# Kernel optimization log

Hardware: AMD Instinct MI355X
Metric: run time of the kernel (lower is better)

The kernel has to match this reference:

```python
import jax, jax.numpy as jnp
import numpy as np
from math import sqrt

B, S, D_MODEL = 2, 2048, 1024
H = 16
ADIM = D_MODEL // H  # 64
K_REL = 16
N_PEMB = 2 * K_REL + 1  # 33, bidirectional rel-pos vocabulary


def setup_inputs() -> dict:
    key = jax.random.key(0)
    ks = jax.random.split(key, 8)
    sc = 0.02
    return {
        "iQ": jax.random.normal(ks[0], (B, S, D_MODEL), jnp.float32),
        "iK": jax.random.normal(ks[1], (B, S, D_MODEL), jnp.float32),
        "iV": jax.random.normal(ks[2], (B, S, D_MODEL), jnp.float32),
        "Wq": jax.random.normal(ks[3], (D_MODEL, D_MODEL), jnp.float32) * sc,
        "Wk": jax.random.normal(ks[4], (D_MODEL, D_MODEL), jnp.float32) * sc,
        "Wv": jax.random.normal(ks[5], (D_MODEL, D_MODEL), jnp.float32) * sc,
        "Wo": jax.random.normal(ks[6], (D_MODEL, D_MODEL), jnp.float32) * sc,
        "rel_pemb": jax.random.normal(ks[7], (N_PEMB, ADIM), jnp.float32) * sc,
    }


def reference(iQ, iK, iV, Wq, Wk, Wv, Wo, rel_pemb):
    b, nq, _ = iQ.shape
    seql = iK.shape[1]
    # projections -> [b, h, len, d]
    q = (iQ @ Wq).reshape(b, nq, H, ADIM).transpose(0, 2, 1, 3)
    k = (iK @ Wk).reshape(b, seql, H, ADIM).transpose(0, 2, 1, 3)
    v = (iV @ Wv).reshape(b, seql, H, ADIM).transpose(0, 2, 1, 3)
    # content scores: [b, h, nq, seql]
    scores = jnp.einsum("bhqd,bhsd->bhqs", q, k)
    # relative position bias: rel[i, j] = clamp(j - i, -K, K) + K
    pos = jnp.arange(seql)
    rel = jnp.clip(pos[None, :] - pos[:, None], -K_REL, K_REL) + K_REL
    rel = rel[seql - nq:, :]  # narrow to query rows: [nq, seql]
    e = rel_pemb[rel]  # [nq, seql, d]
    scores = scores + jnp.einsum("bhqd,qsd->bhqs", q, e)
    scores = scores / sqrt(ADIM)
    attn = jax.nn.softmax(scores, axis=-1)
    ctx = jnp.einsum("bhqs,bhsd->bqhd", attn, v).reshape(b, nq, H * ADIM)
    return ctx @ Wo
```

## Files before the change

kernel.cpp:

```cpp
#include <hip/hip_runtime.h>
#include <hip/hip_bf16.h>

#define BB 2
#define S 2048
#define DM 1024
#define H 16
#define ADIM 64
#define NP 33

typedef __bf16 bf16x8 __attribute__((ext_vector_type(8)));
typedef __bf16 bf16x4 __attribute__((ext_vector_type(4)));
typedef float f32x4 __attribute__((ext_vector_type(4)));

__device__ __forceinline__ void gload16(const void* g, void* l) {
  __builtin_amdgcn_global_load_lds(
      (__attribute__((address_space(1))) void*)(g),
      (__attribute__((address_space(3))) void*)(l), 16, 0, 0);
}

__global__ __launch_bounds__(256) void tobf16(
    const float* __restrict__ X0, const float* __restrict__ X1,
    const float* __restrict__ X2, __bf16* __restrict__ Y0,
    __bf16* __restrict__ Y1, __bf16* __restrict__ Y2) {
  const float* X; __bf16* Y;
  switch (blockIdx.z) {
    case 0: X = X0; Y = Y0; break;
    case 1: X = X1; Y = Y1; break;
    default: X = X2; Y = Y2; break;
  }
  size_t i = ((size_t)blockIdx.x * 256 + threadIdx.x) * 8;
  float4 a0 = *(const float4*)(X + i);
  float4 a1 = *(const float4*)(X + i + 4);
  bf16x8 v;
  v[0] = (__bf16)a0.x; v[1] = (__bf16)a0.y;
  v[2] = (__bf16)a0.z; v[3] = (__bf16)a0.w;
  v[4] = (__bf16)a1.x; v[5] = (__bf16)a1.y;
  v[6] = (__bf16)a1.z; v[7] = (__bf16)a1.w;
  *(bf16x8*)(Y + i) = v;
}

__global__ __launch_bounds__(256) void wtrans(
    const float* __restrict__ W0, const float* __restrict__ W1,
    const float* __restrict__ W2, const float* __restrict__ W3,
    __bf16* __restrict__ T0, __bf16* __restrict__ T1,
    __bf16* __restrict__ T2, __bf16* __restrict__ T3) {
  const float* W; __bf16* T;
  switch (blockIdx.z) {
    case 0: W = W0; T = T0; break;
    case 1: W = W1; T = T1; break;
    case 2: W = W2; T = T2; break;
    default: W = W3; T = T3; break;
  }
  __shared__ __bf16 tile[64][65];
  int j = threadIdx.x & 63, i0 = threadIdx.x >> 6;
  int n0 = blockIdx.x * 64, k0 = blockIdx.y * 64;
#pragma unroll
  for (int p = 0; p < 16; ++p) {
    int i = i0 + p * 4;
    tile[i][j] = (__bf16)W[(size_t)(k0 + i) * DM + n0 + j];
  }
  __syncthreads();
#pragma unroll
  for (int p = 0; p < 16; ++p) {
    int i = i0 + p * 4;
    T[(size_t)(n0 + i) * DM + k0 + j] = tile[j][i];
  }
}

#define LDK 40
template <bool A_FP32, int BN, typename CT>
__device__ __forceinline__ void gemm_body(const void* __restrict__ Av,
                                          const __bf16* __restrict__ BT,
                                          CT* __restrict__ C, int mode,
                                          int m0, int n0) {
  constexpr int NF = BN / 32;
  constexpr int BH = BN / 16;
  __shared__ __align__(16) __bf16 As[128 * LDK];
  __shared__ __align__(16) __bf16 Bs[BN * 32];
  int t = threadIdx.x;
  int w = t >> 6, lane = t & 63, l15 = lane & 15, quad = lane >> 4;
  int wm = w >> 1, wn = w & 1;
  constexpr int LA = A_FP32 ? LDK : 32;
  f32x4 acc[4][NF] = {};
  int lr = t >> 2;
  int lk = (t & 3) * 8;
  int r4 = lane >> 2;
  int c8 = (lane & 3) * 8;
  for (int k0 = 0; k0 < DM; k0 += 32) {
    if constexpr (A_FP32) {
#pragma unroll
      for (int rr = 0; rr < 2; ++rr) {
        int row = rr * 64 + lr;
        const float* src = (const float*)Av + (size_t)(m0 + row) * DM + k0 + lk;
        float4 a0 = *(const float4*)src;
        float4 a1 = *(const float4*)(src + 4);
        bf16x8 v;
        v[0] = (__bf16)a0.x; v[1] = (__bf16)a0.y;
        v[2] = (__bf16)a0.z; v[3] = (__bf16)a0.w;
        v[4] = (__bf16)a1.x; v[5] = (__bf16)a1.y;
        v[6] = (__bf16)a1.z; v[7] = (__bf16)a1.w;
        *(bf16x8*)&As[row * LDK + lk] = v;
      }
    } else {
#pragma unroll
      for (int q = 0; q < 2; ++q) {
        int half = w * 2 + q;
        gload16((const __bf16*)Av + (size_t)(m0 + half * 16 + r4) * DM + k0 + c8,
                &As[half * 512]);
      }
    }
#pragma unroll
    for (int q = 0; q < BH / 4; ++q) {
      int half = w * (BH / 4) + q;
      gload16(&BT[(size_t)(n0 + half * 16 + r4) * DM + k0 + c8],
              &Bs[half * 512]);
    }
    __syncthreads();
    bf16x8 af[4], bfr[NF];
#pragma unroll
    for (int mi = 0; mi < 4; ++mi)
      af[mi] = *(const bf16x8*)&As[(wm * 64 + mi * 16 + l15) * LA + quad * 8];
#pragma unroll
    for (int ni = 0; ni < NF; ++ni)
      bfr[ni] =
          *(const bf16x8*)&Bs[(wn * (BN / 2) + ni * 16 + l15) * 32 + quad * 8];
#pragma unroll
    for (int mi = 0; mi < 4; ++mi)
#pragma unroll
      for (int ni = 0; ni < NF; ++ni)
        acc[mi][ni] = __builtin_amdgcn_mfma_f32_16x16x32_bf16(
            af[mi], bfr[ni], acc[mi][ni], 0, 0, 0);
    __syncthreads();
  }
#pragma unroll
  for (int mi = 0; mi < 4; ++mi)
#pragma unroll
    for (int ni = 0; ni < NF; ++ni)
#pragma unroll
      for (int r = 0; r < 4; ++r) {
        int row = m0 + wm * 64 + mi * 16 + quad * 4 + r;
        int col = n0 + wn * (BN / 2) + ni * 16 + l15;
        CT v = (CT)acc[mi][ni][r];
        if (mode == 0) {
          C[(size_t)row * DM + col] = v;
        } else if (mode == 3) {
          int hh = row >> 6, dd = row & (ADIM - 1);
          int bb = col >> 11, ss = col & (S - 1);
          C[((size_t)(bb * H + hh) * ADIM + dd) * S + ss] = v;
        } else {
          int b = row >> 11, s = row & (S - 1);
          int h = col >> 6, d = col & (ADIM - 1);
          if (mode == 1)
            C[((size_t)(b * H + h) * S + s) * ADIM + d] = v;
          else
            C[((size_t)(b * H + h) * ADIM + d) * S + s] = v;
        }
      }
}

__global__ __launch_bounds__(256) void proj3(
    const float* __restrict__ iQ, const float* __restrict__ iK,
    const float* __restrict__ iV, const __bf16* __restrict__ WqT,
    const __bf16* __restrict__ WkT, const __bf16* __restrict__ WvT,
    __bf16* __restrict__ Qw, __bf16* __restrict__ Kw,
    __bf16* __restrict__ Vt) {
  const float* A; const __bf16* B; __bf16* C; int mode;
  switch (blockIdx.z) {
    case 0: A = iQ; B = WqT; C = Qw; mode = 1; break;
    case 1: A = iK; B = WkT; C = Kw; mode = 1; break;
    default: A = iV; B = WvT; C = Vt; mode = 2; break;
  }
  int i2 = blockIdx.x + (blockIdx.y << 3);
  int xcd = i2 & 7, slot = i2 >> 3;
  int m0 = (xcd + ((slot >> 3) << 3)) * 128;
  int n0 = (slot & 7) * 128;
  gemm_body<true, 128, __bf16>(A, B, C, mode, m0, n0);
}

__global__ __launch_bounds__(256) void proj3b(
    const __bf16* __restrict__ Qb, const __bf16* __restrict__ Kb,
    const __bf16* __restrict__ Vb, const __bf16* __restrict__ WqT,
    const __bf16* __restrict__ WkT, const __bf16* __restrict__ WvT,
    __bf16* __restrict__ Qw, __bf16* __restrict__ Kw,
    __bf16* __restrict__ Vt) {
  int i2 = blockIdx.x + (blockIdx.y << 3);
  if (blockIdx.z == 2) {
    int m0 = (i2 & 7) * 128;
    int n0 = (i2 >> 3) * 128;
    gemm_body<false, 128, __bf16>(WvT, Vb, Vt, 3, m0, n0);
  } else {
    const __bf16* A; const __bf16* B; __bf16* C;
    if (blockIdx.z == 0) { A = Qb; B = WqT; C = Qw; }
    else                 { A = Kb; B = WkT; C = Kw; }
    int xcd = i2 & 7, slot = i2 >> 3;
    int m0 = (xcd + ((slot >> 3) << 3)) * 128;
    int n0 = (slot & 7) * 128;
    gemm_body<false, 128, __bf16>(A, B, C, 1, m0, n0);
  }
}

__global__ __launch_bounds__(256) void gemm_final(
    const __bf16* __restrict__ ctx, const __bf16* __restrict__ WoT,
    float* __restrict__ out) {
  int i2 = blockIdx.x + (blockIdx.y << 4);
  int xcd = i2 & 7, slot = i2 >> 3;
  int m0 = ((xcd << 2) + (slot >> 4)) * 128;
  int n0 = (slot & 15) * 64;
  gemm_body<false, 64, float>(ctx, WoT, out, 0, m0, n0);
}

#define SWZ(row, sl) (((row) << 6) + ((((sl) ^ ((row) & 7))) << 3))
__global__ __launch_bounds__(256) void attn_flash(
    const __bf16* __restrict__ Qw, const __bf16* __restrict__ Kw,
    const __bf16* __restrict__ Vt, const float* __restrict__ pemb,
    __bf16* __restrict__ ctx) {
  int i = blockIdx.x + (blockIdx.y << 5);
  int a = i & 7, j = i >> 3;
  int bh = (a << 2) + (j >> 5);
  int q0 = (j & 31) * 64;
  int b = bh >> 4, h = bh & 15;
  int t = threadIdx.x, w = t >> 6, lane = t & 63, l15 = lane & 15,
      quad = lane >> 4;
  const __bf16* Qh = Qw + (size_t)bh * S * ADIM;
  const __bf16* Kh = Kw + (size_t)bh * S * ADIM;
  const __bf16* Vh = Vt + (size_t)bh * ADIM * S;

  __shared__ __align__(16) char smem[33280];
  __bf16* Ks = (__bf16*)smem;
  __bf16* Vs = (__bf16*)(smem + 8192);
  float* pband = (float*)(smem + 16384);
  __bf16* pbufw = (__bf16*)(smem + 25088 + w * 2048);
  __bf16* peb = (__bf16*)smem;

  for (int ii = t; ii < 48 * 64; ii += 256) {
    int r = ii >> 6, d = ii & 63;
    peb[r * 64 + d] = (r < NP) ? (__bf16)pemb[ii] : (__bf16)0.f;
  }

  int qa = q0 + w * 16 + l15;
  bf16x8 qf0 = *(const bf16x8*)&Qh[(size_t)qa * ADIM + quad * 8];
  bf16x8 qf1 = *(const bf16x8*)&Qh[(size_t)qa * ADIM + 32 + quad * 8];
  __syncthreads();

  {
    f32x4 pc[3] = {};
#pragma unroll
    for (int ni = 0; ni < 3; ++ni) {
      bf16x8 b0 = *(const bf16x8*)&peb[(ni * 16 + l15) * 64 + quad * 8];
      bf16x8 b1 = *(const bf16x8*)&peb[(ni * 16 + l15) * 64 + 32 + quad * 8];
      pc[ni] = __builtin_amdgcn_mfma_f32_16x16x32_bf16(qf0, b0, pc[ni], 0, 0, 0);
      pc[ni] = __builtin_amdgcn_mfma_f32_16x16x32_bf16(qf1, b1, pc[ni], 0, 0, 0);
    }
#pragma unroll
    for (int ni = 0; ni < 3; ++ni)
#pragma unroll
      for (int r = 0; r < 4; ++r) {
        int col = ni * 16 + l15;
        if (col < NP) pband[(w * 16 + quad * 4 + r) * 34 + col] = pc[ni][r];
      }
  }
  __syncthreads();

  int qg = q0 + w * 16 + l15;
  int qc = q0 + w * 16 + quad * 4;
  int qw0 = q0 + w * 16;
  const float* pbrow = pband + (w * 16 + l15) * 34;
  float lsum = 0.f;
  f32x4 o[4] = {};

  float pb0s = pbrow[0] * 0.125f;
  float pb32s = pbrow[32] * 0.125f;

  int srow = t >> 3;
  int sslot = t & 7;
  int scol = sslot * 8;
  bf16x8 k0r = *(const bf16x8*)&Kh[(size_t)srow * ADIM + scol];
  bf16x8 k1r = *(const bf16x8*)&Kh[(size_t)(32 + srow) * ADIM + scol];
  bf16x8 v0r = *(const bf16x8*)&Vh[(size_t)srow * S + scol];
  bf16x8 v1r = *(const bf16x8*)&Vh[(size_t)(32 + srow) * S + scol];

  for (int s0 = 0; s0 < S; s0 += 64) {
    __syncthreads();
    *(bf16x8*)&Ks[SWZ(srow, sslot)] = k0r;
    *(bf16x8*)&Ks[SWZ(32 + srow, sslot)] = k1r;
    *(bf16x8*)&Vs[SWZ(srow, sslot)] = v0r;
    *(bf16x8*)&Vs[SWZ(32 + srow, sslot)] = v1r;
    int sn = s0 + 64;
    if (sn < S) {
      k0r = *(const bf16x8*)&Kh[(size_t)(sn + srow) * ADIM + scol];
      k1r = *(const bf16x8*)&Kh[(size_t)(sn + 32 + srow) * ADIM + scol];
      v0r = *(const bf16x8*)&Vh[(size_t)srow * S + sn + scol];
      v1r = *(const bf16x8*)&Vh[(size_t)(32 + srow) * S + sn + scol];
    }
    __syncthreads();

    f32x4 c[4];
#pragma unroll
    for (int jj = 0; jj < 4; ++jj) {
      f32x4 cj = {};
      int krow = jj * 16 + l15;
      bf16x8 kb0 = *(const bf16x8*)&Ks[SWZ(krow, quad)];
      bf16x8 kb1 = *(const bf16x8*)&Ks[SWZ(krow, 4 + quad)];
      cj = __builtin_amdgcn_mfma_f32_16x16x32_bf16(kb0, qf0, cj, 0, 0, 0);
      cj = __builtin_amdgcn_mfma_f32_16x16x32_bf16(kb1, qf1, cj, 0, 0, 0);
      c[jj] = cj;
    }

    float pv[4][4];
    bool below = (s0 + 79 <= qw0);
    bool above = (s0 >= qw0 + 31);
    if (below || above) {
      float pb = below ? pb0s : pb32s;
#pragma unroll
      for (int jj = 0; jj < 4; ++jj)
#pragma unroll
        for (int r = 0; r < 4; ++r) {
          float e = __expf(__builtin_fmaf(c[jj][r], 0.125f, pb));
          lsum += e;
          pv[jj][r] = e;
        }
    } else {
#pragma unroll
      for (int jj = 0; jj < 4; ++jj)
#pragma unroll
        for (int r = 0; r < 4; ++r) {
          int sg = s0 + jj * 16 + quad * 4 + r;
          int i0 = sg - qg; i0 = i0 < -16 ? -16 : (i0 > 16 ? 16 : i0); i0 += 16;
          float e = __expf((c[jj][r] + pbrow[i0]) * 0.125f);
          lsum += e;
          pv[jj][r] = e;
        }
    }

#pragma unroll
    for (int jj = 0; jj < 4; ++jj) {
      bf16x4 pw;
      pw[0] = (__bf16)pv[jj][0]; pw[1] = (__bf16)pv[jj][1];
      pw[2] = (__bf16)pv[jj][2]; pw[3] = (__bf16)pv[jj][3];
      int sl = (2 * jj + (quad >> 1)) ^ (l15 & 7);
      *(bf16x4*)&pbufw[(l15 << 6) + (sl << 3) + (quad & 1) * 4] = pw;
    }
    bf16x8 pa0 = *(const bf16x8*)&pbufw[SWZ(l15, quad)];
    bf16x8 pa1 = *(const bf16x8*)&pbufw[SWZ(l15, 4 + quad)];

#pragma unroll
    for (int nt = 0; nt < 4; ++nt) {
      int vrow = nt * 16 + l15;
      bf16x8 vb0 = *(const bf16x8*)&Vs[SWZ(vrow, quad)];
      bf16x8 vb1 = *(const bf16x8*)&Vs[SWZ(vrow, 4 + quad)];
      o[nt] = __builtin_amdgcn_mfma_f32_16x16x32_bf16(pa0, vb0, o[nt], 0, 0, 0);
      o[nt] = __builtin_amdgcn_mfma_f32_16x16x32_bf16(pa1, vb1, o[nt], 0, 0, 0);
    }
  }

  lsum += __shfl_xor(lsum, 16, 64);
  lsum += __shfl_xor(lsum, 32, 64);
  float ls[4];
#pragma unroll
  for (int r = 0; r < 4; ++r) ls[r] = __shfl(lsum, quad * 4 + r, 64);
#pragma unroll
  for (int nt = 0; nt < 4; ++nt)
#pragma unroll
    for (int r = 0; r < 4; ++r) {
      int qq = qc + r;
      int d = nt * 16 + l15;
      ctx[(size_t)(b * S + qq) * DM + h * ADIM + d] =
          (__bf16)(o[nt][r] / ls[r]);
    }
}

extern "C" void kernel_launch(void* const* d_in, const int* in_sizes, int n_in,
                              void* d_out, int out_size, void* d_ws,
                              size_t ws_size, hipStream_t stream) {
  bool sizes_ok =
      (n_in == 8 && in_sizes[0] == BB * S * DM && in_sizes[1] == BB * S * DM &&
       in_sizes[2] == BB * S * DM && in_sizes[3] == DM * DM &&
       in_sizes[4] == DM * DM && in_sizes[5] == DM * DM &&
       in_sizes[6] == DM * DM && in_sizes[7] == NP * ADIM &&
       out_size == BB * S * DM);
  if (!sizes_ok) return;
  if (ws_size < 33ull * 1024 * 1024) return;

  const float* iQ = (const float*)d_in[0];
  const float* iK = (const float*)d_in[1];
  const float* iV = (const float*)d_in[2];
  const float* Wq = (const float*)d_in[3];
  const float* Wk = (const float*)d_in[4];
  const float* Wv = (const float*)d_in[5];
  const float* Wo = (const float*)d_in[6];
  const float* pemb = (const float*)d_in[7];

  char* w = (char*)d_ws;
  const size_t MB = 1024 * 1024;
  __bf16* Qw  = (__bf16*)(w + 0 * MB);
  __bf16* Kw  = (__bf16*)(w + 8 * MB);
  __bf16* Vt  = (__bf16*)(w + 16 * MB);
  __bf16* ctx = (__bf16*)(w + 24 * MB);
  __bf16* WqT = (__bf16*)(w + 24 * MB);
  __bf16* WkT = (__bf16*)(w + 26 * MB);
  __bf16* WvT = (__bf16*)(w + 28 * MB);

  bool big = ws_size >= 58ull * 1024 * 1024;
  bool mid = ws_size >= 56ull * 1024 * 1024;
  __bf16* WoT = big ? (__bf16*)(w + 56 * MB) : (__bf16*)(w + 0 * MB);

  if (mid) {
    __bf16* Qb = (__bf16*)(w + 32 * MB);
    __bf16* Kb = (__bf16*)(w + 40 * MB);
    __bf16* Vb = (__bf16*)(w + 48 * MB);
    wtrans<<<dim3(16, 16, big ? 4 : 3), 256, 0, stream>>>(
        Wq, Wk, Wv, Wo, WqT, WkT, WvT, WoT);
    tobf16<<<dim3(2048, 1, 3), 256, 0, stream>>>(iQ, iK, iV, Qb, Kb, Vb);
    proj3b<<<dim3(8, 32, 3), 256, 0, stream>>>(Qb, Kb, Vb, WqT, WkT, WvT,
                                               Qw, Kw, Vt);
    attn_flash<<<dim3(S / 64, BB * H), 256, 0, stream>>>(Qw, Kw, Vt, pemb,
                                                         ctx);
    if (!big)
      wtrans<<<dim3(16, 16, 1), 256, 0, stream>>>(Wo, Wo, Wo, Wo,
                                                  WoT, WoT, WoT, WoT);
  } else {
    wtrans<<<dim3(16, 16, 3), 256, 0, stream>>>(Wq, Wk, Wv, Wq,
                                                WqT, WkT, WvT, WqT);
    proj3<<<dim3(8, 32, 3), 256, 0, stream>>>(iQ, iK, iV, WqT, WkT, WvT,
                                              Qw, Kw, Vt);
    attn_flash<<<dim3(S / 64, BB * H), 256, 0, stream>>>(Qw, Kw, Vt, pemb,
                                                         ctx);
    wtrans<<<dim3(16, 16, 1), 256, 0, stream>>>(Wo, Wo, Wo, Wo,
                                                WoT, WoT, WoT, WoT);
  }
  gemm_final<<<dim3(16, 32), 256, 0, stream>>>(ctx, WoT, (float*)d_out);
}
```

Baseline: 232.9 us.

## Switch attention to 32x32 MFMA with split-KV waves and register P shuffle

The attention kernel now uses 32x32x16 MFMA tiles. The four waves are split into two query halves times two key halves, and the partial outputs and row sums are reduced through shared memory at the end. The P matrix is repacked from the score accumulator layout into A-operand fragments with cross-lane shuffles instead of a per-wave LDS round trip, which shrinks shared memory, and launch bounds request 4 blocks per CU. The aim is fewer MFMA issues and LDS traffic per tile, at the cost of a final cross-wave reduction and higher register pressure.

```diff
diff --git a/kernel.cpp b/kernel.cpp
--- a/kernel.cpp
+++ b/kernel.cpp
@@ -11,11 +11,25 @@
 typedef __bf16 bf16x8 __attribute__((ext_vector_type(8)));
 typedef __bf16 bf16x4 __attribute__((ext_vector_type(4)));
 typedef float f32x4 __attribute__((ext_vector_type(4)));
+typedef float f32x16 __attribute__((ext_vector_type(16)));
 
 __device__ __forceinline__ void gload16(const void* g, void* l) {
   __builtin_amdgcn_global_load_lds(
       (__attribute__((address_space(1))) void*)(g),
       (__attribute__((address_space(3))) void*)(l), 16, 0, 0);
+}
+
+__device__ __forceinline__ unsigned pk2(float a, float b) {
+  unsigned short x = __builtin_bit_cast(unsigned short, (__bf16)a);
+  unsigned short y = __builtin_bit_cast(unsigned short, (__bf16)b);
+  return (unsigned)x | ((unsigned)y << 16);
+}
+__device__ __forceinline__ bf16x8 frag4(unsigned r0, unsigned r1,
+                                        unsigned r2, unsigned r3) {
+  unsigned u[4] = {r0, r1, r2, r3};
+  bf16x8 v;
+  __builtin_memcpy(&v, u, 16);
+  return v;
 }
 
 __global__ __launch_bounds__(256) void tobf16(
@@ -210,7 +224,7 @@
 }
 
 #define SWZ(row, sl) (((row) << 6) + ((((sl) ^ ((row) & 7))) << 3))
-__global__ __launch_bounds__(256) void attn_flash(
+__global__ __launch_bounds__(256, 4) void attn_flash(
     const __bf16* __restrict__ Qw, const __bf16* __restrict__ Kw,
     const __bf16* __restrict__ Vt, const float* __restrict__ pemb,
     __bf16* __restrict__ ctx) {
@@ -219,17 +233,18 @@
   int bh = (a << 2) + (j >> 5);
   int q0 = (j & 31) * 64;
   int b = bh >> 4, h = bh & 15;
-  int t = threadIdx.x, w = t >> 6, lane = t & 63, l15 = lane & 15,
-      quad = lane >> 4;
+  int t = threadIdx.x, w = t >> 6, lane = t & 63;
+  int l31 = lane & 31, hi = lane >> 5;
+  int l15 = lane & 15, quad = lane >> 4;
+  int qh = w & 1, sh = w >> 1;
   const __bf16* Qh = Qw + (size_t)bh * S * ADIM;
   const __bf16* Kh = Kw + (size_t)bh * S * ADIM;
   const __bf16* Vh = Vt + (size_t)bh * ADIM * S;
 
-  __shared__ __align__(16) char smem[33280];
+  __shared__ __align__(16) char smem[25088];
   __bf16* Ks = (__bf16*)smem;
   __bf16* Vs = (__bf16*)(smem + 8192);
   float* pband = (float*)(smem + 16384);
-  __bf16* pbufw = (__bf16*)(smem + 25088 + w * 2048);
   __bf16* peb = (__bf16*)smem;
 
   for (int ii = t; ii < 48 * 64; ii += 256) {
@@ -237,12 +252,11 @@
     peb[r * 64 + d] = (r < NP) ? (__bf16)pemb[ii] : (__bf16)0.f;
   }
 
-  int qa = q0 + w * 16 + l15;
-  bf16x8 qf0 = *(const bf16x8*)&Qh[(size_t)qa * ADIM + quad * 8];
-  bf16x8 qf1 = *(const bf16x8*)&Qh[(size_t)qa * ADIM + 32 + quad * 8];
-  __syncthreads();
-
   {
+    int qa = q0 + w * 16 + l15;
+    bf16x8 qf0 = *(const bf16x8*)&Qh[(size_t)qa * ADIM + quad * 8];
+    bf16x8 qf1 = *(const bf16x8*)&Qh[(size_t)qa * ADIM + 32 + quad * 8];
+    __syncthreads();
     f32x4 pc[3] = {};
 #pragma unroll
     for (int ni = 0; ni < 3; ++ni) {
@@ -261,19 +275,20 @@
   }
   __syncthreads();
 
-  int qg = q0 + w * 16 + l15;
-  int qc = q0 + w * 16 + quad * 4;
-  int qw0 = q0 + w * 16;
-  const float* pbrow = pband + (w * 16 + l15) * 34;
-  float lsum = 0.f;
-  f32x4 o[4] = {};
-
+  int qglob = q0 + qh * 32 + l31;
+  int qwm = q0 + qh * 32;
+  const float* pbrow = pband + (qh * 32 + l31) * 34;
   float pb0s = pbrow[0] * 0.125f;
   float pb32s = pbrow[32] * 0.125f;
-
-  int srow = t >> 3;
-  int sslot = t & 7;
-  int scol = sslot * 8;
+  float lsum = 0.f;
+  f32x16 o0 = {}, o1 = {};
+
+  bf16x8 qfB[4];
+#pragma unroll
+  for (int jk = 0; jk < 4; ++jk)
+    qfB[jk] = *(const bf16x8*)&Qh[(size_t)qglob * ADIM + jk * 16 + hi * 8];
+
+  int srow = t >> 3, sslot = t & 7, scol = sslot * 8;
   bf16x8 k0r = *(const bf16x8*)&Kh[(size_t)srow * ADIM + scol];
   bf16x8 k1r = *(const bf16x8*)&Kh[(size_t)(32 + srow) * ADIM + scol];
   bf16x8 v0r = *(const bf16x8*)&Vh[(size_t)srow * S + scol];
@@ -294,79 +309,92 @@
     }
     __syncthreads();
 
-    f32x4 c[4];
-#pragma unroll
-    for (int jj = 0; jj < 4; ++jj) {
-      f32x4 cj = {};
-      int krow = jj * 16 + l15;
-      bf16x8 kb0 = *(const bf16x8*)&Ks[SWZ(krow, quad)];
-      bf16x8 kb1 = *(const bf16x8*)&Ks[SWZ(krow, 4 + quad)];
-      cj = __builtin_amdgcn_mfma_f32_16x16x32_bf16(kb0, qf0, cj, 0, 0, 0);
-      cj = __builtin_amdgcn_mfma_f32_16x16x32_bf16(kb1, qf1, cj, 0, 0, 0);
-      c[jj] = cj;
-    }
-
-    float pv[4][4];
-    bool below = (s0 + 79 <= qw0);
-    bool above = (s0 >= qw0 + 31);
+    f32x16 c = {};
+    int srowA = sh * 32 + l31;
+#pragma unroll
+    for (int jk = 0; jk < 4; ++jk) {
+      bf16x8 kb = *(const bf16x8*)&Ks[SWZ(srowA, jk * 2 + hi)];
+      c = __builtin_amdgcn_mfma_f32_32x32x16_bf16(kb, qfB[jk], c, 0, 0, 0);
+    }
+
+    bool below = (s0 + sh * 32 + 47 <= qwm);
+    bool above = (s0 + sh * 32 >= qwm + 47);
     if (below || above) {
       float pb = below ? pb0s : pb32s;
 #pragma unroll
-      for (int jj = 0; jj < 4; ++jj)
-#pragma unroll
-        for (int r = 0; r < 4; ++r) {
-          float e = __expf(__builtin_fmaf(c[jj][r], 0.125f, pb));
-          lsum += e;
-          pv[jj][r] = e;
-        }
+      for (int r = 0; r < 16; ++r) {
+        float e = __expf(__builtin_fmaf(c[r], 0.125f, pb));
+        lsum += e;
+        c[r] = e;
+      }
     } else {
 #pragma unroll
-      for (int jj = 0; jj < 4; ++jj)
-#pragma unroll
-        for (int r = 0; r < 4; ++r) {
-          int sg = s0 + jj * 16 + quad * 4 + r;
-          int i0 = sg - qg; i0 = i0 < -16 ? -16 : (i0 > 16 ? 16 : i0); i0 += 16;
-          float e = __expf((c[jj][r] + pbrow[i0]) * 0.125f);
-          lsum += e;
-          pv[jj][r] = e;
-        }
-    }
-
-#pragma unroll
-    for (int jj = 0; jj < 4; ++jj) {
-      bf16x4 pw;
-      pw[0] = (__bf16)pv[jj][0]; pw[1] = (__bf16)pv[jj][1];
-      pw[2] = (__bf16)pv[jj][2]; pw[3] = (__bf16)pv[jj][3];
-      int sl = (2 * jj + (quad >> 1)) ^ (l15 & 7);
-      *(bf16x4*)&pbufw[(l15 << 6) + (sl << 3) + (quad & 1) * 4] = pw;
-    }
-    bf16x8 pa0 = *(const bf16x8*)&pbufw[SWZ(l15, quad)];
-    bf16x8 pa1 = *(const bf16x8*)&pbufw[SWZ(l15, 4 + quad)];
-
-#pragma unroll
-    for (int nt = 0; nt < 4; ++nt) {
-      int vrow = nt * 16 + l15;
-      bf16x8 vb0 = *(const bf16x8*)&Vs[SWZ(vrow, quad)];
-      bf16x8 vb1 = *(const bf16x8*)&Vs[SWZ(vrow, 4 + quad)];
-      o[nt] = __builtin_amdgcn_mfma_f32_16x16x32_bf16(pa0, vb0, o[nt], 0, 0, 0);
-      o[nt] = __builtin_amdgcn_mfma_f32_16x16x32_bf16(pa1, vb1, o[nt], 0, 0, 0);
-    }
-  }
-
-  lsum += __shfl_xor(lsum, 16, 64);
+      for (int r = 0; r < 16; ++r) {
+        int sg = s0 + sh * 32 + (r & 3) + 8 * (r >> 2) + 4 * hi;
+        int i0 = sg - qglob;
+        i0 = i0 < -16 ? -16 : (i0 > 16 ? 16 : i0);
+        i0 += 16;
+        float e = __expf((c[r] + pbrow[i0]) * 0.125f);
+        lsum += e;
+        c[r] = e;
+      }
+    }
+
+    unsigned P01 = pk2(c[0], c[1]), P23 = pk2(c[2], c[3]);
+    unsigned P45 = pk2(c[4], c[5]), P67 = pk2(c[6], c[7]);
+    unsigned P89 = pk2(c[8], c[9]), Pab = pk2(c[10], c[11]);
+    unsigned Pcd = pk2(c[12], c[13]), Pef = pk2(c[14], c[15]);
+    unsigned T01 = (unsigned)__shfl_xor((int)P01, 32, 64);
+    unsigned T23 = (unsigned)__shfl_xor((int)P23, 32, 64);
+    unsigned T45 = (unsigned)__shfl_xor((int)P45, 32, 64);
+    unsigned T67 = (unsigned)__shfl_xor((int)P67, 32, 64);
+    unsigned T89 = (unsigned)__shfl_xor((int)P89, 32, 64);
+    unsigned Tab = (unsigned)__shfl_xor((int)Pab, 32, 64);
+    unsigned Tcd = (unsigned)__shfl_xor((int)Pcd, 32, 64);
+    unsigned Tef = (unsigned)__shfl_xor((int)Pef, 32, 64);
+    bf16x8 pa0 = frag4(hi ? T45 : P01, hi ? T67 : P23,
+                       hi ? P45 : T01, hi ? P67 : T23);
+    bf16x8 pa1 = frag4(hi ? Tcd : P89, hi ? Tef : Pab,
+                       hi ? Pcd : T89, hi ? Pef : Tab);
+
+#pragma unroll
+    for (int jj = 0; jj < 2; ++jj) {
+      bf16x8 paj = jj ? pa1 : pa0;
+      int slot = sh * 4 + jj * 2 + hi;
+      bf16x8 vb0 = *(const bf16x8*)&Vs[SWZ(l31, slot)];
+      bf16x8 vb1 = *(const bf16x8*)&Vs[SWZ(32 + l31, slot)];
+      o0 = __builtin_amdgcn_mfma_f32_32x32x16_bf16(paj, vb0, o0, 0, 0, 0);
+      o1 = __builtin_amdgcn_mfma_f32_32x32x16_bf16(paj, vb1, o1, 0, 0, 0);
+    }
+  }
+
   lsum += __shfl_xor(lsum, 32, 64);
-  float ls[4];
-#pragma unroll
-  for (int r = 0; r < 4; ++r) ls[r] = __shfl(lsum, quad * 4 + r, 64);
-#pragma unroll
-  for (int nt = 0; nt < 4; ++nt)
-#pragma unroll
-    for (int r = 0; r < 4; ++r) {
-      int qq = qc + r;
-      int d = nt * 16 + l15;
-      ctx[(size_t)(b * S + qq) * DM + h * ADIM + d] =
-          (__bf16)(o[nt][r] / ls[r]);
-    }
+  float* Obuf = (float*)smem;
+  float* Lbuf = (float*)(smem + 16384);
+  __syncthreads();
+  if (lane < 32) Lbuf[sh * 64 + qh * 32 + l31] = lsum;
+  if (sh == 1) {
+#pragma unroll
+    for (int r = 0; r < 16; ++r) {
+      int qr = (r & 3) + 8 * (r >> 2) + 4 * hi;
+      Obuf[(qh * 32 + qr) * 64 + l31] = o0[r];
+      Obuf[(qh * 32 + qr) * 64 + 32 + l31] = o1[r];
+    }
+  }
+  __syncthreads();
+  if (sh == 0) {
+#pragma unroll
+    for (int r = 0; r < 16; ++r) {
+      int qr = (r & 3) + 8 * (r >> 2) + 4 * hi;
+      int qloc = qh * 32 + qr;
+      float lt = Lbuf[qloc] + Lbuf[64 + qloc];
+      float t0 = o0[r] + Obuf[qloc * 64 + l31];
+      float t1 = o1[r] + Obuf[qloc * 64 + 32 + l31];
+      size_t base = (size_t)(b * S + q0 + qloc) * DM + h * ADIM;
+      ctx[base + l31] = (__bf16)(t0 / lt);
+      ctx[base + 32 + l31] = (__bf16)(t1 / lt);
+    }
+  }
 }
 
 extern "C" void kernel_launch(void* const* d_in, const int* in_sizes, int n_in,
```

New measurement: 233.0 us. No clear change (+0.0%).
